# Optimization experiments

Hardware: AMD Instinct MI355X
Metric: run time of the kernel (lower is better)

The kernel has to match this reference:

```python
import jax, jax.numpy as jnp
import numpy as np
import math

IN_FEATURES = 4096
OUT_FEATURES = 4096
TOKENS = 8192


def hydrate_weight(seed, out_features, in_features):
    """Deterministically synthesize the virtual weight matrix from the 64-bit seed.
    Mirrors nn.Linear's kaiming-uniform-style bound (1/sqrt(fan_in)) used by gmem_rs
    hydration; never stored as a parameter."""
    bound = 1.0 / math.sqrt(in_features)
    key = jax.random.key(seed)
    return jax.random.uniform(
        key, (out_features, in_features), dtype=jnp.float32,
        minval=-bound, maxval=bound)


def setup_inputs() -> dict:
    key = jax.random.key(0)
    kx, kb = jax.random.split(key)
    x = jax.random.normal(kx, (TOKENS, IN_FEATURES), dtype=jnp.float32)
    bound = 1.0 / math.sqrt(IN_FEATURES)
    bias = jax.random.uniform(kb, (OUT_FEATURES,), dtype=jnp.float32,
                              minval=-bound, maxval=bound)
    return {"x": x, "bias": bias, "seed": 1140071481}


def reference(x, bias, seed):
    # Hydrate weight on-the-fly from seed (zero-RAM virtual weight), then GEMM.
    W = hydrate_weight(seed, OUT_FEATURES, IN_FEATURES)  # [out, in]
    y = jnp.einsum('ti,oi->to', x, W)  # [tokens, out]
    return y + bias
```

## Files before the change

### kernel.cpp

```cpp
#include <hip/hip_runtime.h>
#include <hip/hip_bf16.h>
#include <stdint.h>

#define TOKENS 8192
#define NOUT   4096
#define KIN    4096

#define BM 256
#define BN 256
#define BK 64
#define NT (KIN / BK)

typedef __attribute__((ext_vector_type(8))) short bf16x8;
typedef __attribute__((ext_vector_type(4))) float f32x4;

__device__ __forceinline__ uint32_t rotl32(uint32_t x, int r) {
  return (x << r) | (x >> (32 - r));
}

__device__ __forceinline__ uint16_t f2bf_rne(float f) {
  uint32_t u = __float_as_uint(f);
  u += 0x7FFFu + ((u >> 16) & 1u);
  return (uint16_t)(u >> 16);
}

__device__ __forceinline__ void threefry2x32(uint32_t k0, uint32_t k1,
                                             uint32_t c0, uint32_t c1,
                                             uint32_t& o0, uint32_t& o1) {
  uint32_t ks2 = 0x1BD11BDAu ^ k0 ^ k1;
  uint32_t x0 = c0 + k0;
  uint32_t x1 = c1 + k1;
#define TFR(r) { x0 += x1; x1 = rotl32(x1, (r)); x1 ^= x0; }
  TFR(13) TFR(15) TFR(26) TFR(6)
  x0 += k1;  x1 += ks2 + 1u;
  TFR(17) TFR(29) TFR(16) TFR(24)
  x0 += ks2; x1 += k0 + 2u;
  TFR(13) TFR(15) TFR(26) TFR(6)
  x0 += k0;  x1 += k1 + 3u;
  TFR(17) TFR(29) TFR(16) TFR(24)
  x0 += k1;  x1 += ks2 + 4u;
  TFR(13) TFR(15) TFR(26) TFR(6)
  x0 += ks2; x1 += k0 + 5u;
#undef TFR
  o0 = x0; o1 = x1;
}

__global__ void prep_kernel(const float* __restrict__ x,
                            uint16_t* __restrict__ xb,
                            uint16_t* __restrict__ W,
                            const int* __restrict__ seed_ptr) {
  uint32_t b = blockIdx.x;
  uint32_t g = b / 5u, r = b % 5u;
  if (r < 4u) {
    uint32_t k1 = (uint32_t)(*seed_ptr);
    uint32_t j = (g * 4u + r) * 256u + threadIdx.x;
    uint32_t o0, o1;
    threefry2x32(0u, k1, 0u, j, o0, o1);
    uint32_t bits = o0 ^ o1;
    const float scale = 0.03125f;
    const float mn    = -0.015625f;
    float f = __uint_as_float((bits >> 9) | 0x3F800000u) - 1.0f;
    float v = fmaxf(mn, f * scale + mn);
    W[j] = f2bf_rne(v);
  } else {
    uint32_t base = (g * 256u + threadIdx.x) * 8u;
    f32x4 a = *(const f32x4*)(x + base);
    f32x4 c = *(const f32x4*)(x + base + 4);
    union { uint16_t u[8]; bf16x8 v; } rr;
    rr.u[0] = f2bf_rne(a[0]); rr.u[1] = f2bf_rne(a[1]);
    rr.u[2] = f2bf_rne(a[2]); rr.u[3] = f2bf_rne(a[3]);
    rr.u[4] = f2bf_rne(c[0]); rr.u[5] = f2bf_rne(c[1]);
    rr.u[6] = f2bf_rne(c[2]); rr.u[7] = f2bf_rne(c[3]);
    *(bf16x8*)(xb + base) = rr.v;
  }
}

__global__ __launch_bounds__(512, 2)
void gemm_bias_kernel(const uint16_t* __restrict__ A,
                      const uint16_t* __restrict__ B,
                      const float* __restrict__ bias,
                      float* __restrict__ C) {
  __shared__ uint16_t smem[2][2][16384];

  const int nwgn = NOUT / BN;
  const int nwg  = (TOKENS / BM) * nwgn;
  int bid = blockIdx.x;
  int cpx = nwg >> 3;
  int swzb = (bid & 7) * cpx + (bid >> 3);
  int tm = (swzb / nwgn) * BM;
  int tn = (swzb % nwgn) * BN;

  const int t    = threadIdx.x;
  const int lane = t & 63;
  const int wid  = t >> 6;
  const int wm   = wid >> 2;
  const int wn   = wid & 3;
  const int fr   = lane & 15;
  const int fq   = lane >> 4;

  const int swzRd = (lane & 7) << 4;
  const int lsw   = ((lane & 7) ^ (lane >> 3)) << 4;

  f32x4 acc[8][4] = {};

  auto stageHalf = [&](int mat, int h, int kt, int buf) {
    const uint16_t* g = mat ? B : A;
    const int rb = (mat ? tn : tm) + h * 128 + wid * 16 + (lane >> 3);
    const char* src = (const char*)(g + (size_t)rb * KIN) + kt * 128 + lsw;
    char* dst = (char*)&smem[buf][mat][0] + h * 16384 + wid * 2048 + lane * 16;
#pragma unroll
    for (int q = 0; q < 2; ++q) {
      __builtin_amdgcn_global_load_lds(
          (const __attribute__((address_space(1))) void*)(src + (size_t)q * 8 * KIN * 2),
          (__attribute__((address_space(3))) void*)(dst + q * 1024),
          16, 0, 0);
    }
  };

#define VMW(N) asm volatile("s_waitcnt vmcnt(" #N ")" ::: "memory")
#define LKW(N) asm volatile("s_waitcnt lgkmcnt(" #N ")" ::: "memory")
#define SB0    __builtin_amdgcn_sched_barrier(0)
#define PRI(p) __builtin_amdgcn_s_setprio(p)

#define RD_AS(BUFI, MH, S)                                                     \
    _Pragma("unroll")                                                          \
    for (int i_ = 0; i_ < 4; ++i_)                                             \
      af[S][i_] = *(const bf16x8*)((const char*)&smem[BUFI][0][0] +            \
          (wm * 64 + (MH) * 128 + i_ * 16 + fr) * 128 +                        \
          ((((S) << 6) | (fq << 4)) ^ swzRd));

#define RD_BS(BUFI, BV, NH, S)                                                 \
    _Pragma("unroll")                                                          \
    for (int j_ = 0; j_ < 2; ++j_)                                             \
      BV[S][j_] = *(const bf16x8*)((const char*)&smem[BUFI][1][0] +            \
          (wn * 32 + (NH) * 128 + j_ * 16 + fr) * 128 +                        \
          ((((S) << 6) | (fq << 4)) ^ swzRd));

#define MF8(MH, NH, BV, S)                                                     \
    _Pragma("unroll")                                                          \
    for (int i_ = 0; i_ < 4; ++i_)                                             \
      _Pragma("unroll")                                                        \
      for (int j_ = 0; j_ < 2; ++j_)                                           \
        acc[(MH) * 4 + i_][(NH) * 2 + j_] =                                    \
            __builtin_amdgcn_mfma_f32_16x16x32_bf16(                           \
                af[S][i_], BV[S][j_], acc[(MH) * 4 + i_][(NH) * 2 + j_],       \
                0, 0, 0);

#define KTILE(BUF, KT, MODE)                                                   \
  {                                                                            \
         \
    RD_AS(BUF, 0, 0) RD_BS(BUF, bv0, 0, 0)                                     \
    SB0;                                                                       \
    RD_AS(BUF, 0, 1) RD_BS(BUF, bv0, 0, 1)                                     \
    if ((MODE) <= 1) stageHalf(0, 1, (KT) + 1, (BUF) ^ 1);                     \
    __builtin_amdgcn_s_barrier();                                              \
    LKW(6); SB0; PRI(1); MF8(0, 0, bv0, 0)                                     \
    LKW(0); SB0; MF8(0, 0, bv0, 1) PRI(0);                                     \
                                                \
    RD_BS(BUF, bv1, 1, 0)                                                      \
    SB0;                                                                       \
    RD_BS(BUF, bv1, 1, 1)                                                      \
    __builtin_amdgcn_s_barrier();                                              \
    LKW(2); SB0; PRI(1); MF8(0, 1, bv1, 0)                                     \
    LKW(0); SB0; MF8(0, 1, bv1, 1) PRI(0);                                     \
                       \
    RD_AS(BUF, 1, 0)                                                           \
    SB0;                                                                       \
    RD_AS(BUF, 1, 1)                                                           \
    if ((MODE) == 0) { stageHalf(0, 0, (KT) + 2, (BUF));                       \
                       stageHalf(1, 0, (KT) + 2, (BUF)); }                     \
    __builtin_amdgcn_s_barrier();                                              \
    LKW(4); SB0; PRI(1); MF8(1, 1, bv1, 0)                                     \
    LKW(0); SB0; MF8(1, 1, bv1, 1) PRI(0);                                     \
                   \
    if ((MODE) == 0) stageHalf(1, 1, (KT) + 2, (BUF));                         \
    if ((MODE) == 0) { VMW(6); } else if ((MODE) == 1) { VMW(0); }             \
    __builtin_amdgcn_s_barrier();                                              \
    SB0; PRI(1); MF8(1, 0, bv0, 0) MF8(1, 0, bv0, 1) PRI(0);                   \
  }

  bf16x8 af[2][4], bv0[2][2], bv1[2][2];

  stageHalf(0, 0, 0, 0); stageHalf(1, 0, 0, 0);
  stageHalf(0, 1, 0, 0); stageHalf(1, 1, 0, 0);
  VMW(4);
  stageHalf(0, 0, 1, 1); stageHalf(1, 0, 1, 1); stageHalf(1, 1, 1, 1);
  VMW(6);
  __builtin_amdgcn_s_barrier();

  for (int kt = 0; kt < NT - 2; kt += 2) {
    KTILE(0, kt, 0)
    KTILE(1, kt + 1, 0)
  }
  KTILE(0, 62, 1)
  KTILE(1, 63, 2)

#undef KTILE
#undef MF8
#undef RD_BS
#undef RD_AS
#undef PRI
#undef SB0
#undef LKW
#undef VMW

#pragma unroll
  for (int nj = 0; nj < 4; ++nj) {
    const int nh = nj >> 1, j = nj & 1;
    const int col = tn + wn * 32 + nh * 128 + j * 16 + fr;
    const float bvs = bias[col];
#pragma unroll
    for (int mi = 0; mi < 8; ++mi) {
      const int mh = mi >> 2, i = mi & 3;
      const int row0 = tm + wm * 64 + mh * 128 + i * 16 + fq * 4;
#pragma unroll
      for (int rr = 0; rr < 4; ++rr)
        C[(size_t)(row0 + rr) * NOUT + col] = acc[mi][nj][rr] + bvs;
    }
  }
}

extern "C" void kernel_launch(void* const* d_in, const int* in_sizes, int n_in,
                              void* d_out, int out_size, void* d_ws, size_t ws_size,
                              hipStream_t stream) {
  const float* x    = (const float*)d_in[0];
  const float* bias = (const float*)d_in[1];
  const int*   seed = (const int*)d_in[2];
  float* y = (float*)d_out;

  uint16_t* Wb = (uint16_t*)d_ws;
  uint16_t* Xb = Wb + (size_t)NOUT * KIN;

  prep_kernel<<<81920, 256, 0, stream>>>(x, Xb, Wb, seed);

  const int grid = (TOKENS / BM) * (NOUT / BN);
  gemm_bias_kernel<<<grid, 512, 0, stream>>>(Xb, Wb, bias, y);
}
```

Before: 252.0 us.

## Restructure GEMM k-tile schedule into two barrier phases with precomputed staging pointers

Reorganizes the per-k-tile pipeline from four barrier-separated phases to two. The MFMA sub-blocks are regrouped so that more LDS reads are issued before each compute burst, and the async global-to-LDS prefetches are moved to the new phase boundaries. Staging addresses are precomputed as base pointers that advance per iteration instead of being recomputed in a lambda, which cuts address arithmetic. Fewer barriers reduce synchronization stalls, but keeping more fragments live may raise register pressure, and the changed waitcnt values must exactly match the reordered LDS reads.

New measurement: 259.2 us. 1.03x slower.

```diff
diff --git a/kernel.cpp b/kernel.cpp
--- a/kernel.cpp
+++ b/kernel.cpp
@@ -101,20 +101,23 @@
   const int swzRd = (lane & 7) << 4;
   const int lsw   = ((lane & 7) ^ (lane >> 3)) << 4;
 
+  const char* sA  = (const char*)(A + (size_t)(tm + wid * 16 + (lane >> 3)) * KIN) + lsw;
+  const char* sB  = (const char*)(B + (size_t)(tn + wid * 16 + (lane >> 3)) * KIN) + lsw;
+  const char* sA1 = sA + (size_t)128 * KIN * 2;
+  const char* sB1 = sB + (size_t)128 * KIN * 2;
+
+  char* const dstB = (char*)&smem[0][0][0] + wid * 2048 + lane * 16;
+
   f32x4 acc[8][4] = {};
-
-  auto stageHalf = [&](int mat, int h, int kt, int buf) {
-    const uint16_t* g = mat ? B : A;
-    const int rb = (mat ? tn : tm) + h * 128 + wid * 16 + (lane >> 3);
-    const char* src = (const char*)(g + (size_t)rb * KIN) + kt * 128 + lsw;
-    char* dst = (char*)&smem[buf][mat][0] + h * 16384 + wid * 2048 + lane * 16;
-#pragma unroll
-    for (int q = 0; q < 2; ++q) {
-      __builtin_amdgcn_global_load_lds(
-          (const __attribute__((address_space(1))) void*)(src + (size_t)q * 8 * KIN * 2),
-          (__attribute__((address_space(3))) void*)(dst + q * 1024),
-          16, 0, 0);
-    }
+  bf16x8 af[2][4], bv0[2][2], bv1[2][2];
+
+  auto stage2 = [&](const char* src, char* dst) {
+    __builtin_amdgcn_global_load_lds(
+        (const __attribute__((address_space(1))) void*)src,
+        (__attribute__((address_space(3))) void*)dst, 16, 0, 0);
+    __builtin_amdgcn_global_load_lds(
+        (const __attribute__((address_space(1))) void*)(src + (size_t)8 * KIN * 2),
+        (__attribute__((address_space(3))) void*)(dst + 1024), 16, 0, 0);
   };
 
 #define VMW(N) asm volatile("s_waitcnt vmcnt(" #N ")" ::: "memory")
@@ -146,54 +149,51 @@
                 af[S][i_], BV[S][j_], acc[(MH) * 4 + i_][(NH) * 2 + j_],       \
                 0, 0, 0);
 
-#define KTILE(BUF, KT, MODE)                                                   \
+#define KTILE(BUF, OFF1, OFF2, MODE)                                           \
   {                                                                            \
-         \
+                                                            \
+    __builtin_amdgcn_s_barrier();                                              \
+    if ((MODE) <= 1) stage2(sA1 + (OFF1),                                      \
+                            dstB + ((BUF) ^ 1) * 65536 + 16384);               \
     RD_AS(BUF, 0, 0) RD_BS(BUF, bv0, 0, 0)                                     \
     SB0;                                                                       \
     RD_AS(BUF, 0, 1) RD_BS(BUF, bv0, 0, 1)                                     \
-    if ((MODE) <= 1) stageHalf(0, 1, (KT) + 1, (BUF) ^ 1);                     \
-    __builtin_amdgcn_s_barrier();                                              \
-    LKW(6); SB0; PRI(1); MF8(0, 0, bv0, 0)                                     \
-    LKW(0); SB0; MF8(0, 0, bv0, 1) PRI(0);                                     \
-                                                \
-    RD_BS(BUF, bv1, 1, 0)                                                      \
     SB0;                                                                       \
-    RD_BS(BUF, bv1, 1, 1)                                                      \
-    __builtin_amdgcn_s_barrier();                                              \
-    LKW(2); SB0; PRI(1); MF8(0, 1, bv1, 0)                                     \
-    LKW(0); SB0; MF8(0, 1, bv1, 1) PRI(0);                                     \
-                       \
+    RD_BS(BUF, bv1, 1, 0) RD_BS(BUF, bv1, 1, 1)                                \
+    LKW(10); SB0; PRI(1); MF8(0, 0, bv0, 0)                                    \
+    LKW(4);  SB0; MF8(0, 0, bv0, 1)                                            \
+    LKW(0);  SB0; MF8(0, 1, bv1, 0) MF8(0, 1, bv1, 1) PRI(0);                  \
+                                                            \
     RD_AS(BUF, 1, 0)                                                           \
     SB0;                                                                       \
     RD_AS(BUF, 1, 1)                                                           \
-    if ((MODE) == 0) { stageHalf(0, 0, (KT) + 2, (BUF));                       \
-                       stageHalf(1, 0, (KT) + 2, (BUF)); }                     \
     __builtin_amdgcn_s_barrier();                                              \
-    LKW(4); SB0; PRI(1); MF8(1, 1, bv1, 0)                                     \
-    LKW(0); SB0; MF8(1, 1, bv1, 1) PRI(0);                                     \
-                   \
-    if ((MODE) == 0) stageHalf(1, 1, (KT) + 2, (BUF));                         \
+    if ((MODE) == 0) {                                                         \
+      stage2(sA  + (OFF2), dstB + (BUF) * 65536);                              \
+      stage2(sB  + (OFF2), dstB + (BUF) * 65536 + 32768);                      \
+      stage2(sB1 + (OFF2), dstB + (BUF) * 65536 + 49152);                      \
+    }                                                                          \
+    LKW(4); SB0; PRI(1); MF8(1, 0, bv0, 0)                                     \
+    LKW(0); SB0; MF8(1, 0, bv0, 1) MF8(1, 1, bv1, 0) MF8(1, 1, bv1, 1) PRI(0); \
     if ((MODE) == 0) { VMW(6); } else if ((MODE) == 1) { VMW(0); }             \
-    __builtin_amdgcn_s_barrier();                                              \
-    SB0; PRI(1); MF8(1, 0, bv0, 0) MF8(1, 0, bv0, 1) PRI(0);                   \
-  }
-
-  bf16x8 af[2][4], bv0[2][2], bv1[2][2];
-
-  stageHalf(0, 0, 0, 0); stageHalf(1, 0, 0, 0);
-  stageHalf(0, 1, 0, 0); stageHalf(1, 1, 0, 0);
-  VMW(4);
-  stageHalf(0, 0, 1, 1); stageHalf(1, 0, 1, 1); stageHalf(1, 1, 1, 1);
+  }
+
+  stage2(sA,        dstB);
+  stage2(sB,        dstB + 32768);
+  stage2(sB1,       dstB + 49152);
+  stage2(sA1,       dstB + 16384);
+  stage2(sA  + 128, dstB + 65536);
+  stage2(sB  + 128, dstB + 65536 + 32768);
+  stage2(sB1 + 128, dstB + 65536 + 49152);
   VMW(6);
-  __builtin_amdgcn_s_barrier();
-
-  for (int kt = 0; kt < NT - 2; kt += 2) {
-    KTILE(0, kt, 0)
-    KTILE(1, kt + 1, 0)
-  }
-  KTILE(0, 62, 1)
-  KTILE(1, 63, 2)
+
+  for (int it = 0; it < (NT - 2) / 2; ++it) {
+    KTILE(0, 128, 256, 0)
+    KTILE(1, 256, 384, 0)
+    sA += 256; sB += 256; sA1 += 256; sB1 += 256;
+  }
+  KTILE(0, 128, 0, 1)
+  KTILE(1, 0, 0, 2)
 
 #undef KTILE
 #undef MF8
```
